# Kernel optimization log

Measured on AMD Instinct MI355X. Metric: run time of the kernel, lower is better.

Reference implementation:

```python
import jax, jax.numpy as jnp
import numpy as np

SB_EPSILON = 0.1
SB_SIZE = 1

B, S, L = 16, 256, 24


def _shift(x, axis, k):
    """y[..., i, ...] = x[..., i + k, ...], zero-padded out of range."""
    if k == 0:
        return x
    n = x.shape[axis]
    if k > 0:
        body = jax.lax.slice_in_dim(x, k, n, axis=axis)
        pad = jnp.zeros_like(jax.lax.slice_in_dim(x, 0, k, axis=axis))
        return jnp.concatenate([body, pad], axis=axis)
    k = -k
    body = jax.lax.slice_in_dim(x, 0, n - k, axis=axis)
    pad = jnp.zeros_like(jax.lax.slice_in_dim(x, 0, k, axis=axis))
    return jnp.concatenate([pad, body], axis=axis)


def setup_inputs() -> dict:
    key = jax.random.key(0)
    k1, k2 = jax.random.split(key)
    predict = jax.random.normal(k1, (B, S, S, L), dtype=jnp.float32)
    target = (jax.random.uniform(k2, (B, S, S, L)) < 0.002).astype(jnp.float32)
    # valid spans: end >= start
    tri = (jnp.arange(S)[None, :] >= jnp.arange(S)[:, None]).astype(jnp.int32)
    mask = jnp.broadcast_to(tri[None, :, :, None], (B, S, S, L)).astype(jnp.int32)
    # keep targets only on valid spans
    target = target * mask.astype(jnp.float32)
    return {"predict": predict, "target": target, "mask": mask}


def reference(predict, target, mask):
    dt = predict.dtype
    P = (target == 1).astype(dt)            # positive spans [B,S,S,L]
    M = (mask == 1).astype(dt)              # valid-span mask
    # subtract full epsilon from each positive span
    b2l = jnp.where(target == 1, target - SB_EPSILON, target)
    for dist in range(1, SB_SIZE + 1):
        eps = SB_EPSILON / (SB_SIZE * dist * 4)
        cnt = jnp.zeros_like(P)   # num valid neighbors per positive span
        add = jnp.zeros_like(P)   # smoothing mass scattered onto neighbors
        # NOTE: original code offsets neighbors by sb_size (not dist); identical for sb_size=1
        for axis, k in ((2, SB_SIZE), (2, -SB_SIZE), (1, SB_SIZE), (1, -SB_SIZE)):
            cnt = cnt + _shift(M, axis, k)          # neighbor in range and mask==1
            add = add + _shift(P, axis, -k)         # positives scattering into this cell
        b2l = b2l + eps * (add * M + P * (dist * 4 - cnt))
    # masked BCE-with-logits, mean over mask==1 elements
    x, t = predict, b2l
    bce = jnp.maximum(x, 0) - x * t + jnp.log1p(jnp.exp(-jnp.abs(x)))
    denom = jnp.sum(M)
    return jnp.sum(bce * M) / denom
```

## Files before the change

kernel.cpp:

```cpp
#include <hip/hip_runtime.h>


#define SS 256
#define LL 24

constexpr int   NV4       = 16 * SS * SS * (LL / 4);
constexpr float EPS4      = 0.025f;
constexpr float INV_DENOM = 1.0f / 12632064.0f;
constexpr int   NB        = 2048;
constexpr int   NT        = 256;

__device__ __forceinline__ float bce_term(float x, float t) {
    float ax = fabsf(x);
    return fmaxf(x, 0.f) - x * t + __logf(1.f + __expf(-ax));
}

__global__ __launch_bounds__(NT) void bs_fused(const float4* __restrict__ pred4,
                                               const float4* __restrict__ targ4,
                                               const float*  __restrict__ predf,
                                               float* __restrict__ out) {
    float acc  = 0.f;
    float corr = 0.f;

    for (int q = blockIdx.x * NT + threadIdx.x; q < NV4; q += NB * NT) {
        int cell = q / 6;
        int j = cell & (SS - 1);
        int i = (cell >> 8) & (SS - 1);
        if (j < i) continue;

        float4 x = pred4[q];
        float4 t = targ4[q];

        acc += bce_term(x.x, t.x);
        acc += bce_term(x.y, t.y);
        acc += bce_term(x.z, t.z);
        acc += bce_term(x.w, t.w);

        if (t.x == 1.f || t.y == 1.f || t.z == 1.f || t.w == 1.f) {
            bool hasL = j > i;
            bool hasR = j < SS - 1;
            bool hasU = i > 0;
            float cnt = (hasL ? 2.f : 0.f) + (hasR ? 1.f : 0.f) + (hasU ? 1.f : 0.f);
            int ebase = q * 4;
            float tv[4] = {t.x, t.y, t.z, t.w};
            float xv[4] = {x.x, x.y, x.z, x.w};
#pragma unroll
            for (int k = 0; k < 4; ++k) {
                if (tv[k] == 1.f) {
                    int e = ebase + k;
                    float s = 0.f;
                    if (hasL) s += predf[e - LL];
                    if (hasR) s += predf[e + LL];
                    if (hasU) s += predf[e - LL * SS];
                    if (hasL) s += predf[e + LL * SS];
                    corr += s - xv[k] * cnt;
                }
            }
        }
    }

    float v = fmaf(-EPS4, corr, acc);

#pragma unroll
    for (int off = 32; off; off >>= 1) v += __shfl_down(v, off, 64);
    __shared__ float s[NT / 64];
    int w = threadIdx.x >> 6;
    if ((threadIdx.x & 63) == 0) s[w] = v;
    __syncthreads();
    if (threadIdx.x == 0) {
        float b = 0.f;
#pragma unroll
        for (int k = 0; k < NT / 64; ++k) b += s[k];
        atomicAdd(out, b * INV_DENOM);
    }
}

extern "C" void kernel_launch(void* const* d_in, const int* in_sizes, int n_in,
                              void* d_out, int out_size, void* d_ws, size_t ws_size,
                              hipStream_t stream) {
    const float4* pred4 = (const float4*)d_in[0];
    const float4* targ4 = (const float4*)d_in[1];
    const float*  predf = (const float*)d_in[0];
    float* out = (float*)d_out;

    hipMemsetAsync(out, 0, sizeof(float), stream);
    bs_fused<<<NB, NT, 0, stream>>>(pred4, targ4, predf, out);
}
```

Before: 244.4 us.

## Pair triangular rows per block to iterate only valid upper-triangle spans

Replaces the grid-stride loop over all cells, which filtered out j<i entries per element, with a mapping where each block handles row i and row 255-i of one batch. Together the two rows always hold 257 valid cells, so blocks get equal work and iterate only over upper-triangle float4 vectors. This removes the per-element division and the lanes that were idle on masked cells. The cost is a more rigid decomposition, a tail iteration per block that is only partly filled, and less flexibility in grid size.

```diff
diff --git a/kernel.cpp b/kernel.cpp
--- a/kernel.cpp
+++ b/kernel.cpp
@@ -4,29 +4,34 @@
 #define SS 256
 #define LL 24
 
-constexpr int   NV4       = 16 * SS * SS * (LL / 4);
 constexpr float EPS4      = 0.025f;
 constexpr float INV_DENOM = 1.0f / 12632064.0f;
-constexpr int   NB        = 2048;
 constexpr int   NT        = 256;
+constexpr int   NB        = 16 * 128;
+constexpr int   TOTAL6    = 257 * 6;
 
 __device__ __forceinline__ float bce_term(float x, float t) {
     float ax = fabsf(x);
     return fmaxf(x, 0.f) - x * t + __logf(1.f + __expf(-ax));
 }
 
-__global__ __launch_bounds__(NT) void bs_fused(const float4* __restrict__ pred4,
-                                               const float4* __restrict__ targ4,
-                                               const float*  __restrict__ predf,
-                                               float* __restrict__ out) {
+__global__ __launch_bounds__(NT) void bs_pair(const float4* __restrict__ pred4,
+                                              const float4* __restrict__ targ4,
+                                              const float*  __restrict__ predf,
+                                              float* __restrict__ out) {
+    const int b  = blockIdx.x >> 7;
+    const int iA = blockIdx.x & 127;
+    const int iB = 255 - iA;
+    const int lenA6 = (SS - iA) * 6;
+    const int qA = (((b << 8) + iA) * SS + iA) * 6;
+    const int qB = (((b << 8) + iB) * SS + iB) * 6;
+
     float acc  = 0.f;
     float corr = 0.f;
 
-    for (int q = blockIdx.x * NT + threadIdx.x; q < NV4; q += NB * NT) {
-        int cell = q / 6;
-        int j = cell & (SS - 1);
-        int i = (cell >> 8) & (SS - 1);
-        if (j < i) continue;
+    for (int v = threadIdx.x; v < TOTAL6; v += NT) {
+        bool inA = v < lenA6;
+        int  q   = inA ? (qA + v) : (qB + (v - lenA6));
 
         float4 x = pred4[q];
         float4 t = targ4[q];
@@ -37,6 +42,9 @@
         acc += bce_term(x.w, t.w);
 
         if (t.x == 1.f || t.y == 1.f || t.z == 1.f || t.w == 1.f) {
+            int vloc = inA ? v : (v - lenA6);
+            int i    = inA ? iA : iB;
+            int j    = i + vloc / 6;
             bool hasL = j > i;
             bool hasR = j < SS - 1;
             bool hasU = i > 0;
@@ -59,19 +67,19 @@
         }
     }
 
-    float v = fmaf(-EPS4, corr, acc);
+    float vsum = fmaf(-EPS4, corr, acc);
 
 #pragma unroll
-    for (int off = 32; off; off >>= 1) v += __shfl_down(v, off, 64);
+    for (int off = 32; off; off >>= 1) vsum += __shfl_down(vsum, off, 64);
     __shared__ float s[NT / 64];
     int w = threadIdx.x >> 6;
-    if ((threadIdx.x & 63) == 0) s[w] = v;
+    if ((threadIdx.x & 63) == 0) s[w] = vsum;
     __syncthreads();
     if (threadIdx.x == 0) {
-        float b = 0.f;
+        float bsum = 0.f;
 #pragma unroll
-        for (int k = 0; k < NT / 64; ++k) b += s[k];
-        atomicAdd(out, b * INV_DENOM);
+        for (int k = 0; k < NT / 64; ++k) bsum += s[k];
+        atomicAdd(out, bsum * INV_DENOM);
     }
 }
 
@@ -84,5 +92,5 @@
     float* out = (float*)d_out;
 
     hipMemsetAsync(out, 0, sizeof(float), stream);
-    bs_fused<<<NB, NT, 0, stream>>>(pred4, targ4, predf, out);
+    bs_pair<<<NB, NT, 0, stream>>>(pred4, targ4, predf, out);
 }
```

New measurement: 254.4 us. +4.1%, slower.
